# Kernel optimization log

Measured on AMD Instinct MI355X. Metric: run time of the kernel, lower is better.

The kernel has to match this reference:

```python
import math
import jax, jax.numpy as jnp
import numpy as np

B, N, D, H, PREFIX = 2, 2048, 2048, 16, 512
HD = D // H
ROPE_BASE = 10000.0

def _rope(x):
    # x: [b, h, n, d]; rotate-half RoPE with positions 0..n-1
    d = x.shape[-1]
    n = x.shape[-2]
    inv_freq = 1.0 / (ROPE_BASE ** (jnp.arange(0, d, 2, dtype=jnp.float32) / d))  # [d/2]
    pos = jnp.arange(n, dtype=jnp.float32)
    freqs = pos[:, None] * inv_freq[None, :]            # [n, d/2]
    cos, sin = jnp.cos(freqs), jnp.sin(freqs)
    x1, x2 = x[..., : d // 2], x[..., d // 2 :]
    return jnp.concatenate([x1 * cos - x2 * sin, x2 * cos + x1 * sin], axis=-1).astype(x.dtype)

def setup_inputs() -> dict:
    key = jax.random.key(0)
    ks = jax.random.split(key, 6)
    x = jax.random.normal(ks[0], (B, N, D), dtype=jnp.float32)
    prefix_k = jax.random.normal(ks[1], (B, H, PREFIX, HD), dtype=jnp.float32)
    prefix_v = jax.random.normal(ks[2], (B, H, PREFIX, HD), dtype=jnp.float32)
    Wqkv = jax.random.normal(ks[3], (D, 3 * D), dtype=jnp.float32) * (D ** -0.5)
    bqkv = jnp.zeros((3 * D,), dtype=jnp.float32)
    Wff = jax.random.normal(ks[4], (D, D), dtype=jnp.float32) * (D ** -0.5)
    bff = jnp.zeros((D,), dtype=jnp.float32)
    # causal mask over current tokens; prefix (cache) columns fully visible
    causal = jnp.tril(jnp.ones((N, N), dtype=jnp.int32))
    mask = jnp.concatenate([jnp.ones((N, PREFIX), dtype=jnp.int32), causal], axis=1)[None, None]  # [1,1,N,N+PREFIX]
    return {"x": x, "mask": mask, "prefix_k": prefix_k, "prefix_v": prefix_v,
            "Wqkv": Wqkv, "bqkv": bqkv, "Wff": Wff, "bff": bff}

def reference(x, mask, prefix_k, prefix_v, Wqkv, bqkv, Wff, bff):
    b, n, d = x.shape
    h = prefix_k.shape[1]
    hd = d // h
    qkv = (x @ Wqkv + bqkv).reshape(b, n, 3, h, hd)      # 'b n (c h d)'
    qkv = jnp.transpose(qkv, (2, 0, 3, 1, 4))            # -> c b h n d
    q, k, v = qkv[0], qkv[1], qkv[2]
    k = jnp.concatenate([prefix_k, k], axis=2)           # [b,h,kt,hd]
    v = jnp.concatenate([prefix_v, v], axis=2)
    next_prefix_kv = jnp.stack([k, v])                   # cached BEFORE rope (as in source)
    q = _rope(q)
    k = _rope(k)
    scores = jnp.einsum('bhqd,bhkd->bhqk', q, k) / math.sqrt(hd)
    scores = jnp.where(mask == 0, jnp.finfo(scores.dtype).min, scores)
    probs = jax.nn.softmax(scores, axis=-1)              # dropout_prob=0.0 -> identity
    attn_o = jnp.einsum('bhqk,bhkd->bhqd', probs, v)
    attn_o = jnp.transpose(attn_o, (0, 2, 1, 3)).reshape(b, n, d)
    return attn_o @ Wff + bff, next_prefix_kv
```

## Files before the change

kernel.cpp:

```cpp
#include <hip/hip_runtime.h>
#include <hip/hip_bf16.h>
#include <stdint.h>

#define TPB 256

using f32x4 = __attribute__((ext_vector_type(4))) float;
using s16x8 = __attribute__((ext_vector_type(8))) short;
using s16x4 = __attribute__((ext_vector_type(4))) short;

__device__ __forceinline__ short f2bf(float f){
  union { float f; uint32_t u; } v; v.f = f;
  uint32_t u = v.u;
  uint32_t r = (u + 0x7fffu + ((u >> 16) & 1u)) >> 16;
  return (short)(uint16_t)r;
}
__device__ __forceinline__ float bf2f(short b){
  union { uint32_t u; float f; } v; v.u = ((uint32_t)(uint16_t)b) << 16;
  return v.f;
}
__device__ __forceinline__ f32x4 mfma16(s16x8 a, s16x8 b, f32x4 c){
  return __builtin_amdgcn_mfma_f32_16x16x32_bf16(a, b, c, 0, 0, 0);
}

#define AS1(p) ((const __attribute__((address_space(1))) void*)(p))
#define AS3(p) ((__attribute__((address_space(3))) void*)(p))

__global__ void k_cvt_bf16(const float* __restrict__ src, short* __restrict__ dst, int n8){
  int i = blockIdx.x * TPB + threadIdx.x;
  if (i >= n8) return;
  const float4* s4 = (const float4*)src;
  float4 a = s4[2*i], b = s4[2*i+1];
  s16x8 o;
  o[0]=f2bf(a.x); o[1]=f2bf(a.y); o[2]=f2bf(a.z); o[3]=f2bf(a.w);
  o[4]=f2bf(b.x); o[5]=f2bf(b.y); o[6]=f2bf(b.z); o[7]=f2bf(b.w);
  *(s16x8*)(dst + 8*(size_t)i) = o;
}

__global__ void k_trans_cvt(const float* __restrict__ W, short* __restrict__ WT, int K, int Nn){
  __shared__ float ls[32][33];
  int k0 = blockIdx.x * 32, n0 = blockIdx.y * 32;
  int c = threadIdx.x & 31, i = threadIdx.x >> 5;
#pragma unroll
  for (int rr = 0; rr < 4; rr++){
    int row = i*4 + rr;
    ls[row][c] = W[(size_t)(k0+row)*Nn + n0 + c];
  }
  __syncthreads();
#pragma unroll
  for (int rr = 0; rr < 4; rr++){
    int ro = i*4 + rr;
    WT[(size_t)(n0+ro)*K + k0 + c] = f2bf(ls[c][ro]);
  }
}

template<int EPI>
__global__ void __launch_bounds__(512, 2) k_gemm8(
    const short* __restrict__ A, const short* __restrict__ Bt,
    int Nn, int K,
    const float* __restrict__ bias,
    float* __restrict__ outp,
    float* __restrict__ kvout,
    short* __restrict__ qpre, short* __restrict__ kpre, short* __restrict__ vpre)
{
  __shared__ __align__(16) short As[3][16384];
  __shared__ __align__(16) short Bs[3][8192];
  const int tid = threadIdx.x;
  const int w = tid >> 6, l = tid & 63;
  const int lrow = l & 15, lg = l >> 4;
  const int wm = w >> 1, wn = w & 1;
  const int m0 = blockIdx.x << 8, n0 = blockIdx.y << 7;
  const int NT = K >> 6;

  f32x4 acc[4][4] = {};

#define STAGE_A(slot, t, j) do {                                             \
    int chunk = ((w*4 + (j)) << 6) + l;                                      \
    int row = chunk >> 3, cc = chunk & 7;                                    \
    __builtin_amdgcn_global_load_lds(                                        \
      AS1(A + (size_t)(m0+row)*K + (t)*64 + ((cc ^ (row&7)) << 3)),          \
      AS3(&As[slot][(w*4 + (j)) << 9]), 16, 0, 0);                           \
  } while(0)
#define STAGE_B(slot, t, j) do {                                             \
    int chunk = ((w*2 + (j)) << 6) + l;                                      \
    int row = chunk >> 3, cc = chunk & 7;                                    \
    __builtin_amdgcn_global_load_lds(                                        \
      AS1(Bt + (size_t)(n0+row)*K + (t)*64 + ((cc ^ (row&7)) << 3)),         \
      AS3(&Bs[slot][(w*2 + (j)) << 9]), 16, 0, 0);                           \
  } while(0)

  STAGE_A(0,0,0); STAGE_A(0,0,1); STAGE_A(0,0,2); STAGE_A(0,0,3);
  STAGE_B(0,0,0); STAGE_B(0,0,1);
  STAGE_A(1,1,0); STAGE_A(1,1,1); STAGE_A(1,1,2); STAGE_A(1,1,3);
  STAGE_B(1,1,0); STAGE_B(1,1,1);

  int slot = 0;
  for (int t = 0; t < NT; ++t){
    if (t < NT-1) asm volatile("s_waitcnt vmcnt(6)" ::: "memory");
    else          asm volatile("s_waitcnt vmcnt(0)" ::: "memory");
    __builtin_amdgcn_s_barrier();
    asm volatile("" ::: "memory");
    const int sslot = (slot == 0) ? 2 : slot - 1;
    const bool st = (t+2) < NT;
    const char* ab = (const char*)As[slot];
    const char* bb = (const char*)Bs[slot];

    s16x8 bfr[4][2];
#pragma unroll
    for (int ni = 0; ni < 4; ni++){
      int row = wn*64 + ni*16 + lrow;
#pragma unroll
      for (int ks = 0; ks < 2; ks++)
        bfr[ni][ks] = *(const s16x8*)(bb + row*128 + ((ks*64 + lg*16) ^ ((row&7)<<4)));
    }
    s16x8 af[2][2];
#pragma unroll
    for (int mi = 0; mi < 2; mi++){
      int row = wm*64 + mi*16 + lrow;
#pragma unroll
      for (int ks = 0; ks < 2; ks++)
        af[mi][ks] = *(const s16x8*)(ab + row*128 + ((ks*64 + lg*16) ^ ((row&7)<<4)));
    }
    if (st){ STAGE_A(sslot,t+2,0); STAGE_A(sslot,t+2,1); STAGE_B(sslot,t+2,0); }
    __builtin_amdgcn_s_setprio(1);
#pragma unroll
    for (int ks = 0; ks < 2; ks++)
#pragma unroll
      for (int mi = 0; mi < 2; mi++)
#pragma unroll
        for (int ni = 0; ni < 4; ni++)
          acc[mi][ni] = mfma16(af[mi][ks], bfr[ni][ks], acc[mi][ni]);
    __builtin_amdgcn_s_setprio(0);
    asm volatile("" ::: "memory");
    __builtin_amdgcn_s_barrier();
    asm volatile("" ::: "memory");

    s16x8 af2[2][2];
#pragma unroll
    for (int mi = 0; mi < 2; mi++){
      int row = wm*64 + (mi+2)*16 + lrow;
#pragma unroll
      for (int ks = 0; ks < 2; ks++)
        af2[mi][ks] = *(const s16x8*)(ab + row*128 + ((ks*64 + lg*16) ^ ((row&7)<<4)));
    }
    if (st){ STAGE_A(sslot,t+2,2); STAGE_A(sslot,t+2,3); STAGE_B(sslot,t+2,1); }
    __builtin_amdgcn_s_setprio(1);
#pragma unroll
    for (int ks = 0; ks < 2; ks++)
#pragma unroll
      for (int mi = 0; mi < 2; mi++)
#pragma unroll
        for (int ni = 0; ni < 4; ni++)
          acc[mi+2][ni] = mfma16(af2[mi][ks], bfr[ni][ks], acc[mi+2][ni]);
    __builtin_amdgcn_s_setprio(0);
    slot = (slot == 2) ? 0 : slot + 1;
  }
#undef STAGE_A
#undef STAGE_B

#pragma unroll
  for (int mi = 0; mi < 4; mi++){
#pragma unroll
    for (int ni = 0; ni < 4; ni++){
      const int c  = n0 + wn*64 + ni*16 + lrow;
      const int mb = m0 + wm*64 + mi*16 + lg*4;
      const float bv = bias[c];
      if (EPI == 1){
#pragma unroll
        for (int r = 0; r < 4; r++)
          outp[(size_t)(mb+r)*Nn + c] = acc[mi][ni][r] + bv;
      } else {
        const int s = c >> 11, h = (c >> 7) & 15, tt = c & 127;
#pragma unroll
        for (int r = 0; r < 4; r++){
          const int m = mb + r;
          const int b = m >> 11, n = m & 2047;
          const int bh = b*16 + h;
          const float val = acc[mi][ni][r] + bv;
          if (s == 0){
            qpre[((size_t)bh*2048 + n)*128 + tt] = f2bf(val);
          } else if (s == 1){
            kvout[((size_t)bh*2560 + 512 + n)*128 + tt] = val;
            kpre[((size_t)bh*2048 + n)*128 + tt] = f2bf(val);
          } else {
            kvout[(size_t)(32 + bh)*327680 + (size_t)(512 + n)*128 + tt] = val;
            vpre[((size_t)bh*2048 + n)*128 + tt] = f2bf(val);
          }
        }
      }
    }
  }
}

__global__ void k_rope_q(const short* __restrict__ src, short* __restrict__ dst){
  int gid = blockIdx.x * TPB + threadIdx.x;
  int j = gid & 63; size_t row = gid >> 6;
  int n = (int)(row & 2047);
  float x1 = bf2f(src[row*128 + j]);
  float x2 = bf2f(src[row*128 + 64 + j]);
  float invf = __expf((float)j * (-9.210340371976184f/64.0f));
  float sn, cs; __sincosf((float)n * invf, &sn, &cs);
  const float sc = 0.088388347648318447f;
  dst[row*128 + j]      = f2bf((x1*cs - x2*sn) * sc);
  dst[row*128 + 64 + j] = f2bf((x2*cs + x1*sn) * sc);
}

__global__ void k_rope_k_new(const short* __restrict__ kpre, short* __restrict__ kr){
  int gid = blockIdx.x * TPB + threadIdx.x;
  int j = gid & 63; size_t row = gid >> 6;
  int bh = (int)(row >> 11), n = (int)(row & 2047);
  int pos = 512 + n;
  float x1 = bf2f(kpre[row*128 + j]);
  float x2 = bf2f(kpre[row*128 + 64 + j]);
  float invf = __expf((float)j * (-9.210340371976184f/64.0f));
  float sn, cs; __sincosf((float)pos * invf, &sn, &cs);
  size_t drow = (size_t)bh*2560 + pos;
  kr[drow*128 + j]      = f2bf(x1*cs - x2*sn);
  kr[drow*128 + 64 + j] = f2bf(x2*cs + x1*sn);
}

__global__ void k_rope_k_prefix(const float* __restrict__ pk, float* __restrict__ kvout0,
                                short* __restrict__ kr){
  int gid = blockIdx.x * TPB + threadIdx.x;
  int j = gid & 63; size_t row = gid >> 6;
  int bh = (int)(row >> 9), p = (int)(row & 511);
  float x1 = pk[row*128 + j];
  float x2 = pk[row*128 + 64 + j];
  size_t orow = (size_t)bh*2560 + p;
  kvout0[orow*128 + j]      = x1;
  kvout0[orow*128 + 64 + j] = x2;
  float invf = __expf((float)j * (-9.210340371976184f/64.0f));
  float sn, cs; __sincosf((float)p * invf, &sn, &cs);
  kr[orow*128 + j]      = f2bf(x1*cs - x2*sn);
  kr[orow*128 + 64 + j] = f2bf(x2*cs + x1*sn);
}

__global__ void k_v_prefix(const float* __restrict__ pv, float* __restrict__ kvout1,
                           short* __restrict__ vT){
  __shared__ float ls[32][129];
  int bh = blockIdx.x >> 4, pt = blockIdx.x & 15;
  int p0 = pt*32, tid = threadIdx.x;
#pragma unroll
  for (int i = 0; i < 16; i++){
    int idx = i*TPB + tid; int p = idx >> 7, t = idx & 127;
    float v = pv[((size_t)bh*512 + p0 + p)*128 + t];
    ls[p][t] = v;
    kvout1[((size_t)bh*2560 + p0 + p)*128 + t] = v;
  }
  __syncthreads();
#pragma unroll
  for (int i = 0; i < 16; i++){
    int idx = i*TPB + tid; int t = idx >> 5, p = idx & 31;
    vT[((size_t)bh*128 + t)*2560 + p0 + p] = f2bf(ls[p][t]);
  }
}

__global__ void k_v_new(const short* __restrict__ vpre, short* __restrict__ vT){
  __shared__ float ls[32][129];
  int bh = blockIdx.x >> 6, nt = blockIdx.x & 63;
  int n0 = nt*32, tid = threadIdx.x;
#pragma unroll
  for (int i = 0; i < 16; i++){
    int idx = i*TPB + tid; int p = idx >> 7, t = idx & 127;
    ls[p][t] = bf2f(vpre[((size_t)bh*2048 + n0 + p)*128 + t]);
  }
  __syncthreads();
#pragma unroll
  for (int i = 0; i < 16; i++){
    int idx = i*TPB + tid; int t = idx >> 5, p = idx & 31;
    vT[((size_t)bh*128 + t)*2560 + 512 + n0 + p] = f2bf(ls[p][t]);
  }
}

__global__ void __launch_bounds__(256, 2) k_attn(
    const short* __restrict__ qr, const short* __restrict__ kr,
    const short* __restrict__ vT, short* __restrict__ attno)
{
  __shared__ short Ks[2][64*128];
  __shared__ short VTs[2][128*64];
  __shared__ short Ps[4][16*64];
  const int bh = blockIdx.x;
  const int pA = blockIdx.y, pB = 31 - pA;
  const int nA = 9 + pA, nTot = 49;
  const int tid = threadIdx.x, w = tid >> 6, l = tid & 63;
  const int lrow = l & 15, lg = l >> 4;
  const int b = bh >> 4, h = bh & 15;

  s16x8 qfA[4], qfB[4];
  {
    const size_t rA = (size_t)bh*2048 + pA*64 + w*16 + lrow;
    const size_t rB = (size_t)bh*2048 + pB*64 + w*16 + lrow;
#pragma unroll
    for (int ks = 0; ks < 4; ks++){
      qfA[ks] = *(const s16x8*)&qr[rA*128 + ks*32 + lg*8];
      qfB[ks] = *(const s16x8*)&qr[rB*128 + ks*32 + lg*8];
    }
  }

#define STAGE_KV(buf, kv0s) do {                                                    \
    _Pragma("unroll")                                                               \
    for (int i_ = 0; i_ < 4; i_++){                                                 \
      int chunk = i_*256 + tid;                                                     \
      int row = chunk >> 4, cc = (chunk & 15) ^ (row & 7);                          \
      __builtin_amdgcn_global_load_lds(                                             \
        AS1(kr + ((size_t)bh*2560 + (kv0s) + row)*128 + cc*8),                      \
        AS3((char*)Ks[buf] + (i_*256 + w*64)*16), 16, 0, 0);                        \
    }                                                                               \
    _Pragma("unroll")                                                               \
    for (int i_ = 0; i_ < 4; i_++){                                                 \
      int chunk = i_*256 + tid;                                                     \
      int row = chunk >> 3, cc = (chunk & 7) ^ (row & 7);                           \
      __builtin_amdgcn_global_load_lds(                                             \
        AS1(vT + ((size_t)bh*128 + row)*2560 + (kv0s) + cc*8),                      \
        AS3((char*)VTs[buf] + (i_*256 + w*64)*16), 16, 0, 0);                       \
    }                                                                               \
  } while(0)

  STAGE_KV(0, 0);
  STAGE_KV(1, 64);

  char* psw = (char*)&Ps[w][0];
  int g = 0;
#pragma unroll 2
  for (int ph = 0; ph < 2; ph++){
    const int qt = ph ? pB : pA;
    const int n = 9 + qt;
    const int qbw = qt*64 + w*16;
    f32x4 acc[8] = {};
    float mr = -1e30f, lsum = 0.f;

    for (int t = 0; t < n; t++, g++){
      if (g+1 < nTot) asm volatile("s_waitcnt vmcnt(8)" ::: "memory");
      else            asm volatile("s_waitcnt vmcnt(0)" ::: "memory");
      __builtin_amdgcn_s_barrier();
      asm volatile("" ::: "memory");
      const char* kb_ = (const char*)Ks[g&1];
      const char* vb_ = (const char*)VTs[g&1];
      const int kv0 = t*64;

      f32x4 sf[4];
      __builtin_amdgcn_s_setprio(1);
#pragma unroll
      for (int kb = 0; kb < 4; kb++){
        f32x4 s = {0.f,0.f,0.f,0.f};
#pragma unroll
        for (int ks = 0; ks < 4; ks++){
          int row  = kb*16 + lrow;
          int colb = ks*64 + lg*16;
          s16x8 kf = *(const s16x8*)(kb_ + row*256 + (colb ^ ((row&7)<<4)));
          s = mfma16(kf, ph ? qfB[ks] : qfA[ks], s);
        }
        sf[kb] = s;
      }
      __builtin_amdgcn_s_setprio(0);

      const int qme = 512 + qbw + lrow;
      if (kv0 + 63 > 512 + qbw){
#pragma unroll
        for (int kb = 0; kb < 4; kb++)
#pragma unroll
          for (int r = 0; r < 4; r++){
            int kg = kv0 + kb*16 + lg*4 + r;
            if (kg > qme) sf[kb][r] = -1e30f;
          }
      }

      float m_ = fmaxf(
          fmaxf(fmaxf(fmaxf(sf[0][0],sf[0][1]),fmaxf(sf[0][2],sf[0][3])),
                fmaxf(fmaxf(sf[1][0],sf[1][1]),fmaxf(sf[1][2],sf[1][3]))),
          fmaxf(fmaxf(fmaxf(sf[2][0],sf[2][1]),fmaxf(sf[2][2],sf[2][3])),
                fmaxf(fmaxf(sf[3][0],sf[3][1]),fmaxf(sf[3][2],sf[3][3]))));
      m_ = fmaxf(m_, __shfl_xor(m_, 16));
      m_ = fmaxf(m_, __shfl_xor(m_, 32));

      if (__any(m_ > mr + 8.f)){
        float mnew = fmaxf(mr, m_);
        float sc = __expf(mr - mnew);
        mr = mnew;
        lsum *= sc;
        float scr[4];
#pragma unroll
        for (int r = 0; r < 4; r++)
          scr[r] = __shfl(sc, (l & 48) | (lg*4 + r));
#pragma unroll
        for (int dt = 0; dt < 8; dt++)
#pragma unroll
          for (int r = 0; r < 4; r++) acc[dt][r] *= scr[r];
      }

#pragma unroll
      for (int kb = 0; kb < 4; kb++){
        float p0 = __expf(sf[kb][0] - mr);
        float p1 = __expf(sf[kb][1] - mr);
        float p2 = __expf(sf[kb][2] - mr);
        float p3 = __expf(sf[kb][3] - mr);
        lsum += (p0+p1)+(p2+p3);
        s16x4 pk4 = { f2bf(p0), f2bf(p1), f2bf(p2), f2bf(p3) };
        *(s16x4*)(psw + (lrow*128 + ((kb*32 + lg*8) ^ ((lrow&7)<<4)))) = pk4;
      }

      __builtin_amdgcn_s_setprio(1);
#pragma unroll
      for (int kp = 0; kp < 2; kp++){
        s16x8 pa = *(const s16x8*)(psw + (lrow*128 + ((kp*64 + lg*16) ^ ((lrow&7)<<4))));
#pragma unroll
        for (int dt = 0; dt < 8; dt++){
          int vrow = dt*16 + lrow;
          int vcolb = kp*64 + lg*16;
          s16x8 vf = *(const s16x8*)(vb_ + vrow*128 + (vcolb ^ ((vrow&7)<<4)));
          acc[dt] = mfma16(pa, vf, acc[dt]);
        }
      }
      __builtin_amdgcn_s_setprio(0);

      asm volatile("" ::: "memory");
      __builtin_amdgcn_s_barrier();
      asm volatile("" ::: "memory");
      const int gg = g + 2;
      if (gg < nTot){
        const int kvs = (gg < nA ? gg : gg - nA) * 64;
        STAGE_KV(g&1, kvs);
      }
    }

    float ls_ = lsum;
    ls_ += __shfl_xor(ls_, 16);
    ls_ += __shfl_xor(ls_, 32);
    float linv[4];
#pragma unroll
    for (int r = 0; r < 4; r++)
      linv[r] = 1.f / __shfl(ls_, (l & 48) | (lg*4 + r));
#pragma unroll
    for (int dt = 0; dt < 8; dt++){
#pragma unroll
      for (int r = 0; r < 4; r++){
        int nrow = qbw + lg*4 + r;
        int dcol = h*128 + dt*16 + lrow;
        attno[((size_t)b*2048 + nrow)*2048 + dcol] = f2bf(acc[dt][r] * linv[r]);
      }
    }
  }
#undef STAGE_KV
}

extern "C" void kernel_launch(void* const* d_in, const int* in_sizes, int n_in,
                              void* d_out, int out_size, void* d_ws, size_t ws_size,
                              hipStream_t stream)
{
  const float* x    = (const float*)d_in[0];
  const float* pk   = (const float*)d_in[2];
  const float* pv   = (const float*)d_in[3];
  const float* Wqkv = (const float*)d_in[4];
  const float* bqkv = (const float*)d_in[5];
  const float* Wff  = (const float*)d_in[6];
  const float* bff  = (const float*)d_in[7];
  float* out   = (float*)d_out;
  float* kvout = out + 8388608;

  char* ws = (char*)d_ws;
  short* xb    = (short*)(ws);
  short* wqkvT = (short*)(ws + 16777216);
  short* wffT  = (short*)(ws + 41943040);
  short* qpre  = (short*)(ws + 50331648);
  short* kpre  = (short*)(ws + 67108864);
  short* vpre  = (short*)(ws + 83886080);
  short* qrp   = (short*)(ws + 100663296);
  short* krp   = (short*)(ws + 117440512);
  short* vTp   = (short*)(ws + 138412032);
  short* attno = (short*)(ws + 159383552);

  k_cvt_bf16<<<4096, TPB, 0, stream>>>(x, xb, 1048576);
  k_trans_cvt<<<dim3(64, 192), TPB, 0, stream>>>(Wqkv, wqkvT, 2048, 6144);
  k_trans_cvt<<<dim3(64, 64),  TPB, 0, stream>>>(Wff,  wffT,  2048, 2048);

  k_gemm8<0><<<dim3(16, 48), 512, 0, stream>>>(xb, wqkvT, 6144, 2048, bqkv,
                                               nullptr, kvout, qpre, kpre, vpre);

  k_rope_q<<<16384, TPB, 0, stream>>>(qpre, qrp);
  k_rope_k_new<<<16384, TPB, 0, stream>>>(kpre, krp);
  k_rope_k_prefix<<<4096, TPB, 0, stream>>>(pk, kvout, krp);
  k_v_prefix<<<512, TPB, 0, stream>>>(pv, kvout + (size_t)32*327680, vTp);
  k_v_new<<<2048, TPB, 0, stream>>>(vpre, vTp);

  k_attn<<<dim3(32, 16), TPB, 0, stream>>>(qrp, krp, vTp, attno);

  k_gemm8<1><<<dim3(16, 16), 512, 0, stream>>>(attno, wffT, 2048, 2048, bff,
                                               out, nullptr, nullptr, nullptr, nullptr);
}
```

Measured before the change: 315.7 us.

## Use 256x256 tile GEMM for QKV projection with split-phase pipelined loads

Replaces the QKV projection GEMM with a new kernel using 256x256 output tiles, 384 blocks of 512 threads, an 8x4 wave layout and 128x64 per-wave accumulators. The load of the stage two steps ahead is split into two halves that are interleaved with the two halves of the MFMA work. Bigger tiles raise arithmetic intensity and cut global/L2 traffic for the x and W operands. In exchange, accumulator register pressure rises and the grid gets coarser, about 1.5 waves of blocks on the CUs.

```diff
diff --git a/kernel.cpp b/kernel.cpp
--- a/kernel.cpp
+++ b/kernel.cpp
@@ -50,6 +50,128 @@
   for (int rr = 0; rr < 4; rr++){
     int ro = i*4 + rr;
     WT[(size_t)(n0+ro)*K + k0 + c] = f2bf(ls[c][ro]);
+  }
+}
+
+__global__ void __launch_bounds__(512, 2) k_gemm16(
+    const short* __restrict__ A, const short* __restrict__ Bt,
+    const float* __restrict__ bias,
+    float* __restrict__ kvout,
+    short* __restrict__ qpre, short* __restrict__ kpre, short* __restrict__ vpre)
+{
+  __shared__ __align__(16) short As[3][8192];
+  __shared__ __align__(16) short Bs[3][8192];
+  const int tid = threadIdx.x;
+  const int w = tid >> 6, l = tid & 63;
+  const int lrow = l & 15, lg = l >> 4;
+  const int wm = w >> 2, wn = w & 3;
+  const int lid = blockIdx.x + (int)gridDim.x * blockIdx.y;
+  const int swz = (lid & 7) * 48 + (lid >> 3);
+  const int m0 = (swz & 15) << 8, n0 = (swz >> 4) << 8;
+  constexpr int NT = 64;
+
+  f32x4 acc[8][4] = {};
+
+  size_t offA0, offA1, offB0, offB1;
+  {
+    const int s0 = tid, s1 = 512 + tid;
+    const int gr0 = ((s0 >> 6) << 4) + (s0 & 15), c80 = ((s0 >> 4) & 3) * 8;
+    const int gr1 = ((s1 >> 6) << 4) + (s1 & 15), c81 = ((s1 >> 4) & 3) * 8;
+    offA0 = (size_t)(m0 + gr0) * 2048 + c80;
+    offA1 = (size_t)(m0 + gr1) * 2048 + c81;
+    offB0 = (size_t)(n0 + gr0) * 2048 + c80;
+    offB1 = (size_t)(n0 + gr1) * 2048 + c81;
+  }
+  const int dst0 = w * 1024;
+  const int dst1 = 8192 + w * 1024;
+
+#define STG_A0(sl, t_) __builtin_amdgcn_global_load_lds(AS1(A  + offA0 + (size_t)(t_)*32), AS3((char*)As[sl] + dst0), 16, 0, 0)
+#define STG_A1(sl, t_) __builtin_amdgcn_global_load_lds(AS1(A  + offA1 + (size_t)(t_)*32), AS3((char*)As[sl] + dst1), 16, 0, 0)
+#define STG_B0(sl, t_) __builtin_amdgcn_global_load_lds(AS1(Bt + offB0 + (size_t)(t_)*32), AS3((char*)Bs[sl] + dst0), 16, 0, 0)
+#define STG_B1(sl, t_) __builtin_amdgcn_global_load_lds(AS1(Bt + offB1 + (size_t)(t_)*32), AS3((char*)Bs[sl] + dst1), 16, 0, 0)
+
+  STG_A0(0,0); STG_A1(0,0); STG_B0(0,0); STG_B1(0,0);
+  STG_A0(1,1); STG_A1(1,1); STG_B0(1,1); STG_B1(1,1);
+
+  const int rdo  = lg * 256 + lrow * 16;
+  const int aoff = wm * 8192 + rdo;
+  const int boff = wn * 4096 + rdo;
+
+  int slot = 0;
+  for (int t = 0; t < NT; ++t){
+    if (t < NT-1) asm volatile("s_waitcnt vmcnt(4)" ::: "memory");
+    else          asm volatile("s_waitcnt vmcnt(0)" ::: "memory");
+    __builtin_amdgcn_s_barrier();
+    asm volatile("" ::: "memory");
+    const int sslot = (slot == 0) ? 2 : slot - 1;
+    const bool st = (t+2) < NT;
+    const char* ab = (const char*)As[slot];
+    const char* bb = (const char*)Bs[slot];
+
+    s16x8 bfr[4];
+#pragma unroll
+    for (int ni = 0; ni < 4; ni++)
+      bfr[ni] = *(const s16x8*)(bb + boff + ni*1024);
+    s16x8 af[4];
+#pragma unroll
+    for (int mi = 0; mi < 4; mi++)
+      af[mi] = *(const s16x8*)(ab + aoff + mi*1024);
+    if (st){ STG_A0(sslot, t+2); STG_B0(sslot, t+2); }
+    __builtin_amdgcn_s_setprio(1);
+#pragma unroll
+    for (int mi = 0; mi < 4; mi++)
+#pragma unroll
+      for (int ni = 0; ni < 4; ni++)
+        acc[mi][ni] = mfma16(af[mi], bfr[ni], acc[mi][ni]);
+    __builtin_amdgcn_s_setprio(0);
+    asm volatile("" ::: "memory");
+    __builtin_amdgcn_s_barrier();
+    asm volatile("" ::: "memory");
+
+    s16x8 af2[4];
+#pragma unroll
+    for (int mi = 0; mi < 4; mi++)
+      af2[mi] = *(const s16x8*)(ab + aoff + (mi+4)*1024);
+    if (st){ STG_A1(sslot, t+2); STG_B1(sslot, t+2); }
+    __builtin_amdgcn_s_setprio(1);
+#pragma unroll
+    for (int mi = 0; mi < 4; mi++)
+#pragma unroll
+      for (int ni = 0; ni < 4; ni++)
+        acc[mi+4][ni] = mfma16(af2[mi], bfr[ni], acc[mi+4][ni]);
+    __builtin_amdgcn_s_setprio(0);
+    slot = (slot == 2) ? 0 : slot + 1;
+  }
+#undef STG_A0
+#undef STG_A1
+#undef STG_B0
+#undef STG_B1
+
+#pragma unroll
+  for (int mi = 0; mi < 8; mi++){
+#pragma unroll
+    for (int ni = 0; ni < 4; ni++){
+      const int c  = n0 + wn*64 + ni*16 + lrow;
+      const int mb = m0 + wm*128 + mi*16 + lg*4;
+      const float bv = bias[c];
+      const int s = c >> 11, h = (c >> 7) & 15, tt = c & 127;
+#pragma unroll
+      for (int r = 0; r < 4; r++){
+        const int m = mb + r;
+        const int b = m >> 11, n = m & 2047;
+        const int bh = b*16 + h;
+        const float val = acc[mi][ni][r] + bv;
+        if (s == 0){
+          qpre[((size_t)bh*2048 + n)*128 + tt] = f2bf(val);
+        } else if (s == 1){
+          kvout[((size_t)bh*2560 + 512 + n)*128 + tt] = val;
+          kpre[((size_t)bh*2048 + n)*128 + tt] = f2bf(val);
+        } else {
+          kvout[(size_t)(32 + bh)*327680 + (size_t)(512 + n)*128 + tt] = val;
+          vpre[((size_t)bh*2048 + n)*128 + tt] = f2bf(val);
+        }
+      }
+    }
   }
 }
 
@@ -472,8 +594,7 @@
   k_trans_cvt<<<dim3(64, 192), TPB, 0, stream>>>(Wqkv, wqkvT, 2048, 6144);
   k_trans_cvt<<<dim3(64, 64),  TPB, 0, stream>>>(Wff,  wffT,  2048, 2048);
 
-  k_gemm8<0><<<dim3(16, 48), 512, 0, stream>>>(xb, wqkvT, 6144, 2048, bqkv,
-                                               nullptr, kvout, qpre, kpre, vpre);
+  k_gemm16<<<dim3(16, 24), 512, 0, stream>>>(xb, wqkvT, bqkv, kvout, qpre, kpre, vpre);
 
   k_rope_q<<<16384, TPB, 0, stream>>>(qpre, qrp);
   k_rope_k_new<<<16384, TPB, 0, stream>>>(kpre, krp);
```

Result: slower. 351.1 us (+11.2%).

## Replace 256x128 GEMM with 128x128 tiles, K-step 32, and XCD-aware block swizzle

Applied to the files above, without the earlier changes.

Both projection GEMMs move from a 512-thread, 256x128-tile kernel with K-step 64 and split-phase MFMA loops to a 256-thread, 128x128-tile kernel with K-step 32. Tiles are staged into LDS already in MFMA-fragment order, so each wave reads fragments with plain contiguous offsets and needs no XOR swizzle or mid-iteration barrier. Block IDs are remapped so neighbouring tiles are spread across XCDs. The aim is more resident workgroups (three per CU) and simpler, conflict-free LDS reads. The cost is less operand reuse per tile and more global traffic per FLOP.

```diff
diff --git a/kernel.cpp b/kernel.cpp
--- a/kernel.cpp
+++ b/kernel.cpp
@@ -54,7 +54,7 @@
 }
 
 template<int EPI>
-__global__ void __launch_bounds__(512, 2) k_gemm8(
+__global__ void __launch_bounds__(256, 3) k_gemm128(
     const short* __restrict__ A, const short* __restrict__ Bt,
     int Nn, int K,
     const float* __restrict__ bias,
@@ -62,100 +62,77 @@
     float* __restrict__ kvout,
     short* __restrict__ qpre, short* __restrict__ kpre, short* __restrict__ vpre)
 {
-  __shared__ __align__(16) short As[3][16384];
-  __shared__ __align__(16) short Bs[3][8192];
+  __shared__ __align__(16) short As[3][4096];
+  __shared__ __align__(16) short Bs[3][4096];
   const int tid = threadIdx.x;
   const int w = tid >> 6, l = tid & 63;
   const int lrow = l & 15, lg = l >> 4;
   const int wm = w >> 1, wn = w & 1;
-  const int m0 = blockIdx.x << 8, n0 = blockIdx.y << 7;
-  const int NT = K >> 6;
+  const int nwg = (int)(gridDim.x * gridDim.y);
+  const int lid = (int)blockIdx.x + (int)gridDim.x * (int)blockIdx.y;
+  const int swz = (lid & 7) * (nwg >> 3) + (lid >> 3);
+  const int m0 = (swz & 31) << 7, n0 = (swz >> 5) << 7;
+  const int NT = K >> 5;
 
   f32x4 acc[4][4] = {};
 
-#define STAGE_A(slot, t, j) do {                                             \
-    int chunk = ((w*4 + (j)) << 6) + l;                                      \
-    int row = chunk >> 3, cc = chunk & 7;                                    \
-    __builtin_amdgcn_global_load_lds(                                        \
-      AS1(A + (size_t)(m0+row)*K + (t)*64 + ((cc ^ (row&7)) << 3)),          \
-      AS3(&As[slot][(w*4 + (j)) << 9]), 16, 0, 0);                           \
+  const int rA0 = ((tid >> 6) << 4) + (tid & 15), cA0 = ((tid >> 4) & 3) << 3;
+  const int s1  = 256 + tid;
+  const int rA1 = ((s1 >> 6) << 4) + (s1 & 15),  cA1 = ((s1 >> 4) & 3) << 3;
+  const size_t offA0 = (size_t)(m0 + rA0) * K + cA0;
+  const size_t offA1 = (size_t)(m0 + rA1) * K + cA1;
+  const size_t offB0 = (size_t)(n0 + rA0) * K + cA0;
+  const size_t offB1 = (size_t)(n0 + rA1) * K + cA1;
+  const int d0 = tid * 16, d1 = (256 + tid) * 16;
+
+#define STG(sl, t_) do {                                                          \
+    __builtin_amdgcn_global_load_lds(AS1(A  + offA0 + (size_t)(t_)*32),           \
+                                     AS3((char*)As[sl] + d0), 16, 0, 0);          \
+    __builtin_amdgcn_global_load_lds(AS1(A  + offA1 + (size_t)(t_)*32),           \
+                                     AS3((char*)As[sl] + d1), 16, 0, 0);          \
+    __builtin_amdgcn_global_load_lds(AS1(Bt + offB0 + (size_t)(t_)*32),           \
+                                     AS3((char*)Bs[sl] + d0), 16, 0, 0);          \
+    __builtin_amdgcn_global_load_lds(AS1(Bt + offB1 + (size_t)(t_)*32),           \
+                                     AS3((char*)Bs[sl] + d1), 16, 0, 0);          \
   } while(0)
-#define STAGE_B(slot, t, j) do {                                             \
-    int chunk = ((w*2 + (j)) << 6) + l;                                      \
-    int row = chunk >> 3, cc = chunk & 7;                                    \
-    __builtin_amdgcn_global_load_lds(                                        \
-      AS1(Bt + (size_t)(n0+row)*K + (t)*64 + ((cc ^ (row&7)) << 3)),         \
-      AS3(&Bs[slot][(w*2 + (j)) << 9]), 16, 0, 0);                           \
-  } while(0)
-
-  STAGE_A(0,0,0); STAGE_A(0,0,1); STAGE_A(0,0,2); STAGE_A(0,0,3);
-  STAGE_B(0,0,0); STAGE_B(0,0,1);
-  STAGE_A(1,1,0); STAGE_A(1,1,1); STAGE_A(1,1,2); STAGE_A(1,1,3);
-  STAGE_B(1,1,0); STAGE_B(1,1,1);
+
+  STG(0, 0);
+  STG(1, 1);
+
+  const int rdo  = lg * 256 + lrow * 16;
+  const int aoff = wm * 4096 + rdo;
+  const int boff = wn * 4096 + rdo;
 
   int slot = 0;
   for (int t = 0; t < NT; ++t){
-    if (t < NT-1) asm volatile("s_waitcnt vmcnt(6)" ::: "memory");
+    if (t < NT-1) asm volatile("s_waitcnt vmcnt(4)" ::: "memory");
     else          asm volatile("s_waitcnt vmcnt(0)" ::: "memory");
     __builtin_amdgcn_s_barrier();
     asm volatile("" ::: "memory");
     const int sslot = (slot == 0) ? 2 : slot - 1;
-    const bool st = (t+2) < NT;
     const char* ab = (const char*)As[slot];
     const char* bb = (const char*)Bs[slot];
-
-    s16x8 bfr[4][2];
-#pragma unroll
-    for (int ni = 0; ni < 4; ni++){
-      int row = wn*64 + ni*16 + lrow;
-#pragma unroll
-      for (int ks = 0; ks < 2; ks++)
-        bfr[ni][ks] = *(const s16x8*)(bb + row*128 + ((ks*64 + lg*16) ^ ((row&7)<<4)));
-    }
-    s16x8 af[2][2];
-#pragma unroll
-    for (int mi = 0; mi < 2; mi++){
-      int row = wm*64 + mi*16 + lrow;
-#pragma unroll
-      for (int ks = 0; ks < 2; ks++)
-        af[mi][ks] = *(const s16x8*)(ab + row*128 + ((ks*64 + lg*16) ^ ((row&7)<<4)));
-    }
-    if (st){ STAGE_A(sslot,t+2,0); STAGE_A(sslot,t+2,1); STAGE_B(sslot,t+2,0); }
+    if (t + 2 < NT) STG(sslot, t+2);
+
+    s16x8 af[4], bfr[4];
+#pragma unroll
+    for (int mi = 0; mi < 4; mi++)
+      af[mi] = *(const s16x8*)(ab + aoff + mi*1024);
+#pragma unroll
+    for (int ni = 0; ni < 4; ni++)
+      bfr[ni] = *(const s16x8*)(bb + boff + ni*1024);
+
     __builtin_amdgcn_s_setprio(1);
 #pragma unroll
-    for (int ks = 0; ks < 2; ks++)
-#pragma unroll
-      for (int mi = 0; mi < 2; mi++)
-#pragma unroll
-        for (int ni = 0; ni < 4; ni++)
-          acc[mi][ni] = mfma16(af[mi][ks], bfr[ni][ks], acc[mi][ni]);
+    for (int mi = 0; mi < 4; mi++)
+#pragma unroll
+      for (int ni = 0; ni < 4; ni++)
+        acc[mi][ni] = mfma16(af[mi], bfr[ni], acc[mi][ni]);
     __builtin_amdgcn_s_setprio(0);
-    asm volatile("" ::: "memory");
-    __builtin_amdgcn_s_barrier();
-    asm volatile("" ::: "memory");
-
-    s16x8 af2[2][2];
-#pragma unroll
-    for (int mi = 0; mi < 2; mi++){
-      int row = wm*64 + (mi+2)*16 + lrow;
-#pragma unroll
-      for (int ks = 0; ks < 2; ks++)
-        af2[mi][ks] = *(const s16x8*)(ab + row*128 + ((ks*64 + lg*16) ^ ((row&7)<<4)));
-    }
-    if (st){ STAGE_A(sslot,t+2,2); STAGE_A(sslot,t+2,3); STAGE_B(sslot,t+2,1); }
-    __builtin_amdgcn_s_setprio(1);
-#pragma unroll
-    for (int ks = 0; ks < 2; ks++)
-#pragma unroll
-      for (int mi = 0; mi < 2; mi++)
-#pragma unroll
-        for (int ni = 0; ni < 4; ni++)
-          acc[mi+2][ni] = mfma16(af2[mi][ks], bfr[ni][ks], acc[mi+2][ni]);
-    __builtin_amdgcn_s_setprio(0);
+
     slot = (slot == 2) ? 0 : slot + 1;
   }
-#undef STAGE_A
-#undef STAGE_B
+#undef STG
 
 #pragma unroll
   for (int mi = 0; mi < 4; mi++){
@@ -472,8 +449,8 @@
   k_trans_cvt<<<dim3(64, 192), TPB, 0, stream>>>(Wqkv, wqkvT, 2048, 6144);
   k_trans_cvt<<<dim3(64, 64),  TPB, 0, stream>>>(Wff,  wffT,  2048, 2048);
 
-  k_gemm8<0><<<dim3(16, 48), 512, 0, stream>>>(xb, wqkvT, 6144, 2048, bqkv,
-                                               nullptr, kvout, qpre, kpre, vpre);
+  k_gemm128<0><<<dim3(32, 48), 256, 0, stream>>>(xb, wqkvT, 6144, 2048, bqkv,
+                                                 nullptr, kvout, qpre, kpre, vpre);
 
   k_rope_q<<<16384, TPB, 0, stream>>>(qpre, qrp);
   k_rope_k_new<<<16384, TPB, 0, stream>>>(kpre, krp);
@@ -483,6 +460,6 @@
 
   k_attn<<<dim3(32, 16), TPB, 0, stream>>>(qrp, krp, vTp, attno);
 
-  k_gemm8<1><<<dim3(16, 16), 512, 0, stream>>>(attno, wffT, 2048, 2048, bff,
-                                               out, nullptr, nullptr, nullptr, nullptr);
-}
+  k_gemm128<1><<<dim3(32, 16), 256, 0, stream>>>(attno, wffT, 2048, 2048, bff,
+                                                 out, nullptr, nullptr, nullptr, nullptr);
+}
```

Result: slower. 433.1 us (+37.2%).
